# Kernel tuning notes

Hardware: AMD Instinct MI355X
Metric: run time of the kernel (lower is better)

Reference implementation:

```python
import jax, jax.numpy as jnp
import numpy as np

NUM_HEADS = 16
HEAD_DIM = 80
DIM = NUM_HEADS * HEAD_DIM
SEQ = 2048
SCALE = HEAD_DIM ** -0.5


def rotate_half(x):
    x1, x2 = jnp.split(x, 2, axis=-1)
    return jnp.concatenate((-x2, x1), axis=-1)


def setup_inputs() -> dict:
    key = jax.random.key(0)
    ks = jax.random.split(key, 8)
    hidden_states = jax.random.normal(ks[0], (SEQ, DIM), dtype=jnp.float32)
    cu_seqlens = jnp.array([0, SEQ], dtype=jnp.int32)  # unused by the math
    # rotary embeddings for head_dim
    inv_freq = 1.0 / (10000.0 ** (jnp.arange(0, HEAD_DIM // 2, dtype=jnp.float32) / (HEAD_DIM // 2)))
    freqs = jnp.outer(jnp.arange(SEQ, dtype=jnp.float32), inv_freq)  # [S, hd/2]
    emb = jnp.concatenate((freqs, freqs), axis=-1)  # [S, hd]
    cos = jnp.cos(emb)
    sin = jnp.sin(emb)
    w_qkv = jax.random.normal(ks[1], (3 * DIM, DIM), dtype=jnp.float32) * (DIM ** -0.5)
    b_qkv = jax.random.normal(ks[2], (3 * DIM,), dtype=jnp.float32) * 0.02
    w_proj = jax.random.normal(ks[3], (DIM, DIM), dtype=jnp.float32) * (DIM ** -0.5)
    b_proj = jax.random.normal(ks[4], (DIM,), dtype=jnp.float32) * 0.02
    return {"hidden_states": hidden_states, "cu_seqlens": cu_seqlens, "cos": cos,
            "sin": sin, "w_qkv": w_qkv, "b_qkv": b_qkv, "w_proj": w_proj, "b_proj": b_proj}


def reference(hidden_states, cu_seqlens, cos, sin, w_qkv, b_qkv, w_proj, b_proj):
    S = hidden_states.shape[0]
    qkv = hidden_states @ w_qkv.T + b_qkv  # [S, 3*D]
    qkv = qkv.reshape(S, 3, NUM_HEADS, HEAD_DIM)
    q, k, v = qkv[:, 0], qkv[:, 1], qkv[:, 2]  # each [S, H, hd]
    c = cos[:, None, :]  # [S, 1, hd]
    s = sin[:, None, :]
    q = q * c + rotate_half(q) * s
    k = k * c + rotate_half(k) * s
    # SDPA, non-causal: [H, S, S]
    scores = jnp.einsum('shd,thd->hst', q, k) * SCALE
    attn = jax.nn.softmax(scores, axis=-1)
    out = jnp.einsum('hst,thd->shd', attn, v).reshape(S, DIM)
    return out @ w_proj.T + b_proj
```

## Files before the change

kernel.cpp:

```cpp
#include <hip/hip_runtime.h>


#define SEQLEN   2048
#define DIMM     1280
#define NHEADS   16
#define HD       80
#define QKV_N    3840
#define NSPLIT   4
#define KVSPAN   (SEQLEN / NSPLIT)
#define QSCALE_LOG2E 0.16130083587064776f

#define KSTRIDE  88
#define VFSTRIDE 24

#define EXP2F(x) __builtin_amdgcn_exp2f(x)

#define GLD16(gptr, lptr)                                                      \
    __builtin_amdgcn_global_load_lds(                                          \
        (const __attribute__((address_space(1))) void*)(gptr),                 \
        (__attribute__((address_space(3))) void*)(lptr), 16, 0, 0)

typedef float f32x4 __attribute__((ext_vector_type(4)));
typedef _Float16 half8 __attribute__((ext_vector_type(8)));
typedef _Float16 half4 __attribute__((ext_vector_type(4)));
typedef _Float16 half2v __attribute__((ext_vector_type(2)));

static __device__ __forceinline__ f32x4 mfma_16x16x32(half8 a, half8 b, f32x4 c) {
    return __builtin_amdgcn_mfma_f32_16x16x32_f16(a, b, c, 0, 0, 0);
}
static __device__ __forceinline__ f32x4 mfma_16x16x16(half4 a, half4 b, f32x4 c) {
    return __builtin_amdgcn_mfma_f32_16x16x16f16(a, b, c, 0, 0, 0);
}
static __device__ __forceinline__ half4 lo4(half8 v) {
    return __builtin_shufflevector(v, v, 0, 1, 2, 3);
}
static __device__ __forceinline__ half4 hi4(half8 v) {
    return __builtin_shufflevector(v, v, 4, 5, 6, 7);
}

__global__ __launch_bounds__(256)
void cast_all(const float* __restrict__ hs, const float* __restrict__ wq,
              const float* __restrict__ wp, _Float16* __restrict__ dhs,
              _Float16* __restrict__ dwq, _Float16* __restrict__ dwp) {
    const int n1 = SEQLEN * DIMM / 4, n2 = QKV_N * DIMM / 4, n3 = DIMM * DIMM / 4;
    int i = blockIdx.x * 256 + threadIdx.x;
    const float4* src; half4* dst; int j;
    if (i < n1)           { src = (const float4*)hs; dst = (half4*)dhs; j = i; }
    else if (i < n1 + n2) { src = (const float4*)wq; dst = (half4*)dwq; j = i - n1; }
    else if (i < n1 + n2 + n3) { src = (const float4*)wp; dst = (half4*)dwp; j = i - n1 - n2; }
    else return;
    const float4 v = src[j];
    half4 h;
    h.x = (_Float16)v.x; h.y = (_Float16)v.y;
    h.z = (_Float16)v.z; h.w = (_Float16)v.w;
    dst[j] = h;
}

template<bool OUT_F16>
__global__ __launch_bounds__(512, 4)
void gemm_bt128(const _Float16* __restrict__ A, const _Float16* __restrict__ B,
                const float* __restrict__ bias, void* __restrict__ Cout,
                int M, int N, int K) {
    __shared__ __align__(16) _Float16 As[2][128 * 32];
    __shared__ __align__(16) _Float16 Bs[2][128 * 32];
    const int tid  = threadIdx.x;
    const int lane = tid & 63;
    const int wave = tid >> 6;
    const int l15  = lane & 15;
    const int quad = lane >> 4;
    const int wm   = wave & 3;
    const int wn   = wave >> 2;
    const long bm = blockIdx.x, bn = blockIdx.y;

    const _Float16* Ag = A + bm * 128 * (long)K;
    const _Float16* Bg = B + bn * 128 * (long)K;

    const int srow = lane >> 2;
    const int scol = (lane & 3) * 8;
    f32x4 acc[2][4] = {};

    for (int k0 = 0; k0 < K; k0 += 64) {
        __syncthreads();
#pragma unroll
        for (int p = 0; p < 2; p++) {
            const int kp = k0 + p * 32;
            const long r = 16 * wave + srow;
            GLD16(Ag + r * K + kp + scol, &As[p][512 * wave + lane * 8]);
            GLD16(Bg + r * K + kp + scol, &Bs[p][512 * wave + lane * 8]);
        }
        __syncthreads();
#pragma unroll
        for (int p = 0; p < 2; p++) {
            half8 af[2], bf[4];
#pragma unroll
            for (int t = 0; t < 2; t++)
                af[t] = *(const half8*)&As[p][(wm * 32 + t * 16 + l15) * 32 + quad * 8];
#pragma unroll
            for (int t = 0; t < 4; t++)
                bf[t] = *(const half8*)&Bs[p][(wn * 64 + t * 16 + l15) * 32 + quad * 8];
#pragma unroll
            for (int mt = 0; mt < 2; mt++)
#pragma unroll
                for (int nt = 0; nt < 4; nt++)
                    acc[mt][nt] = mfma_16x16x32(af[mt], bf[nt], acc[mt][nt]);
        }
    }

    float bv[4];
#pragma unroll
    for (int nt = 0; nt < 4; nt++)
        bv[nt] = bias[bn * 128 + wn * 64 + nt * 16 + l15];

#pragma unroll
    for (int mt = 0; mt < 2; mt++) {
#pragma unroll
        for (int r = 0; r < 4; r++) {
            const long row = bm * 128 + wm * 32 + mt * 16 + quad * 4 + r;
#pragma unroll
            for (int nt = 0; nt < 4; nt++) {
                const long col = bn * 128 + wn * 64 + nt * 16 + l15;
                const float v = acc[mt][nt][r] + bv[nt];
                if (OUT_F16) ((_Float16*)Cout)[row * (long)N + col] = (_Float16)v;
                else         ((float*)Cout)[row * (long)N + col] = v;
            }
        }
    }
}

template<bool OUT_F16>
__global__ __launch_bounds__(256, 2)
void gemm_bt64(const _Float16* __restrict__ A, const _Float16* __restrict__ B,
               const float* __restrict__ bias, void* __restrict__ Cout,
               int M, int N, int K) {
    __shared__ __align__(16) _Float16 As[2][64 * 32];
    __shared__ __align__(16) _Float16 Bs[2][128 * 32];
    const int tid  = threadIdx.x;
    const int lane = tid & 63;
    const int wave = tid >> 6;
    const int l15  = lane & 15;
    const int quad = lane >> 4;
    const int wm   = wave & 1;
    const int wn   = wave >> 1;
    const long bm = blockIdx.x, bn = blockIdx.y;

    const _Float16* Ag = A + bm * 64 * (long)K;
    const _Float16* Bg = B + bn * 128 * (long)K;

    const int srow = lane >> 2;
    const int scol = (lane & 3) * 8;
    f32x4 acc[2][4] = {};

    for (int k0 = 0; k0 < K; k0 += 64) {
        __syncthreads();
#pragma unroll
        for (int p = 0; p < 2; p++) {
            const int kp = k0 + p * 32;
            const long arow = 16 * wave + srow;
            GLD16(Ag + arow * K + kp + scol, &As[p][512 * wave + lane * 8]);
#pragma unroll
            for (int cc = 0; cc < 2; cc++) {
                const int c = wave + cc * 4;
                const long brow = 16 * c + srow;
                GLD16(Bg + brow * K + kp + scol, &Bs[p][512 * c + lane * 8]);
            }
        }
        __syncthreads();
#pragma unroll
        for (int p = 0; p < 2; p++) {
            half8 af[2], bf[4];
#pragma unroll
            for (int t = 0; t < 2; t++)
                af[t] = *(const half8*)&As[p][(wm * 32 + t * 16 + l15) * 32 + quad * 8];
#pragma unroll
            for (int t = 0; t < 4; t++)
                bf[t] = *(const half8*)&Bs[p][(wn * 64 + t * 16 + l15) * 32 + quad * 8];
#pragma unroll
            for (int mt = 0; mt < 2; mt++)
#pragma unroll
                for (int nt = 0; nt < 4; nt++)
                    acc[mt][nt] = mfma_16x16x32(af[mt], bf[nt], acc[mt][nt]);
        }
    }

    float bv[4];
#pragma unroll
    for (int nt = 0; nt < 4; nt++)
        bv[nt] = bias[bn * 128 + wn * 64 + nt * 16 + l15];

#pragma unroll
    for (int mt = 0; mt < 2; mt++) {
#pragma unroll
        for (int r = 0; r < 4; r++) {
            const long row = bm * 64 + wm * 32 + mt * 16 + quad * 4 + r;
#pragma unroll
            for (int nt = 0; nt < 4; nt++) {
                const long col = bn * 128 + wn * 64 + nt * 16 + l15;
                const float v = acc[mt][nt][r] + bv[nt];
                if (OUT_F16) ((_Float16*)Cout)[row * (long)N + col] = (_Float16)v;
                else         ((float*)Cout)[row * (long)N + col] = v;
            }
        }
    }
}

__global__ __launch_bounds__(256)
void rope_repack_t(const _Float16* __restrict__ qkv,
                   const float* __restrict__ cosb,
                   const float* __restrict__ sinb,
                   _Float16* __restrict__ Qh,
                   _Float16* __restrict__ Kh,
                   _Float16* __restrict__ Vt) {
    const int s0 = blockIdx.x * 64;
    const int h  = blockIdx.y;
    __shared__ __align__(16) _Float16 Ts[64 * 88];
    const int tid = threadIdx.x;

    for (int i = tid; i < 640; i += 256) {
        const int r = i / 10, c = (i - r * 10) * 8;
        *(half8*)&Ts[r * 88 + c] =
            *(const half8*)&qkv[(long)(s0 + r) * QKV_N + 2 * DIMM + h * HD + c];
    }

    for (int i = tid; i < 320; i += 256) {
        const int r = i / 5, d = (i - r * 5) * 8;
        const _Float16* row = qkv + (long)(s0 + r) * QKV_N + h * HD;
        const half8 q0 = *(const half8*)&row[d];
        const half8 q1 = *(const half8*)&row[d + 40];
        const half8 k0 = *(const half8*)&row[DIMM + d];
        const half8 k1 = *(const half8*)&row[DIMM + d + 40];
        const float4 cA = *(const float4*)&cosb[(s0 + r) * HD + d];
        const float4 cB = *(const float4*)&cosb[(s0 + r) * HD + d + 4];
        const float4 sA = *(const float4*)&sinb[(s0 + r) * HD + d];
        const float4 sB = *(const float4*)&sinb[(s0 + r) * HD + d + 4];
        half8 qo0, qo1, ko0, ko1;
#pragma unroll
        for (int j = 0; j < 8; j++) {
            const float cj = (j < 4) ? cA[j] : cB[j - 4];
            const float sj = (j < 4) ? sA[j] : sB[j - 4];
            qo0[j] = (_Float16)(((float)q0[j] * cj - (float)q1[j] * sj) * QSCALE_LOG2E);
            qo1[j] = (_Float16)(((float)q1[j] * cj + (float)q0[j] * sj) * QSCALE_LOG2E);
            ko0[j] = (_Float16)((float)k0[j] * cj - (float)k1[j] * sj);
            ko1[j] = (_Float16)((float)k1[j] * cj + (float)k0[j] * sj);
        }
        const long o = ((long)h * SEQLEN + s0 + r) * HD;
        *(half8*)&Qh[o + d]      = qo0;
        *(half8*)&Qh[o + d + 40] = qo1;
        *(half8*)&Kh[o + d]      = ko0;
        *(half8*)&Kh[o + d + 40] = ko1;
    }
    __syncthreads();
    for (int i = tid; i < 640; i += 256) {
        const int d = i >> 3, sc = (i & 7) * 8;
        half8 v;
#pragma unroll
        for (int j = 0; j < 8; j++) v[j] = Ts[(sc + j) * 88 + d];
        *(half8*)&Vt[((long)h * HD + d) * SEQLEN + s0 + sc] = v;
    }
}

__global__ __launch_bounds__(512, 4)
void attn_kernel(const _Float16* __restrict__ Qh, const _Float16* __restrict__ Kh,
                 const _Float16* __restrict__ Vt,
                 _Float16* __restrict__ Ohat0, _Float16* __restrict__ Ohat1,
                 float* __restrict__ Lpart) {
    const int s0 = blockIdx.x * 256;
    const int h  = blockIdx.y;
    const int z  = blockIdx.z;
    __shared__ __align__(16) _Float16 Ks[64 * KSTRIDE];
    __shared__ __align__(16) _Float16 VF[5 * 64 * VFSTRIDE];

    const int tid  = threadIdx.x;
    const int lane = tid & 63;
    const int wave = tid >> 6;
    const int l15  = lane & 15;
    const int quad = lane >> 4;

    const int zBeg = z * KVSPAN, zEnd = zBeg + KVSPAN;

    const _Float16* Qg0 = Qh + ((long)h * SEQLEN + s0 + wave * 32 + l15) * HD;
    const _Float16* Qg1 = Qg0 + 16 * (long)HD;
    const half8 qA0 = *(const half8*)&Qg0[quad * 8];
    const half8 qA1 = *(const half8*)&Qg0[32 + quad * 8];
    const half4 qA2 = *(const half4*)&Qg0[64 + quad * 4];
    const half8 qB0 = *(const half8*)&Qg1[quad * 8];
    const half8 qB1 = *(const half8*)&Qg1[32 + quad * 8];
    const half4 qB2 = *(const half4*)&Qg1[64 + quad * 4];

    int offA, dsA, offB, dsB0, dsB1 = 0, offC = 0, dsC0 = 0, dsC1 = 0;
    {
        const int rA = tid / 10, cA = (tid - rA * 10) * 8;
        offA = rA * HD + cA;
        dsA  = rA * KSTRIDE + cA;
        if (tid < 128) {
            const int cB = tid + 512;
            const int rB = cB / 10, ccB = (cB - rB * 10) * 8;
            offB = rB * HD + ccB;
            dsB0 = rB * KSTRIDE + ccB;
        } else {
            const int v = tid - 128, d = v >> 3, c8 = (v & 7) * 8;
            offB = d * SEQLEN + c8;
            const int nt = d >> 4, ld = d & 15, ct = c8 >> 4, qb = (c8 & 15) >> 2;
            dsB0 = (nt * 64 + qb * 16 + ld) * VFSTRIDE + ct * 4;
            dsB1 = (nt * 64 + (qb + 1) * 16 + ld) * VFSTRIDE + ct * 4;
        }
        if (tid < 256) {
            const int v = tid + 384, d = v >> 3, c8 = (v & 7) * 8;
            offC = d * SEQLEN + c8;
            const int nt = d >> 4, ld = d & 15, ct = c8 >> 4, qb = (c8 & 15) >> 2;
            dsC0 = (nt * 64 + qb * 16 + ld) * VFSTRIDE + ct * 4;
            dsC1 = (nt * 64 + (qb + 1) * 16 + ld) * VFSTRIDE + ct * 4;
        }
    }
    const _Float16* KzBase = Kh + ((long)h * SEQLEN + zBeg) * HD;
    const _Float16* VzBase = Vt + (long)h * HD * SEQLEN + zBeg;

    f32x4 oaccA[5] = {}, oaccB[5] = {};
    float laA0 = 0.f, laA1 = 0.f, laB0 = 0.f, laB1 = 0.f;
    const half2v ones2 = {(_Float16)1.f, (_Float16)1.f};

    for (int t0 = zBeg; t0 < zEnd; t0 += 64) {
        const _Float16* KzT = KzBase + (long)(t0 - zBeg) * HD;
        const _Float16* VzT = VzBase + (t0 - zBeg);
        const half8 a = *(const half8*)(KzT + offA);
        half8 b;
        if (tid < 128) b = *(const half8*)(KzT + offB);
        else           b = *(const half8*)(VzT + offB);
        half8 cv = {};
        if (tid < 256) cv = *(const half8*)(VzT + offC);

        __syncthreads();
        *(half8*)&Ks[dsA] = a;
        if (tid < 128) { *(half8*)&Ks[dsB0] = b; }
        else {
            *(half4*)&VF[dsB0] = lo4(b);
            *(half4*)&VF[dsB1] = hi4(b);
        }
        if (tid < 256) {
            *(half4*)&VF[dsC0] = lo4(cv);
            *(half4*)&VF[dsC1] = hi4(cv);
        }
        __syncthreads();

        f32x4 saA[4] = {}, saB[4] = {};
        __builtin_amdgcn_s_setprio(1);
#pragma unroll
        for (int ct = 0; ct < 4; ct++) {
            const int kb = (ct * 16 + l15) * KSTRIDE;
            const half8 kf0 = *(const half8*)&Ks[kb + quad * 8];
            const half8 kf1 = *(const half8*)&Ks[kb + 32 + quad * 8];
            const half4 kf2 = *(const half4*)&Ks[kb + 64 + quad * 4];
            saA[ct] = mfma_16x16x32(kf0, qA0, saA[ct]);
            saB[ct] = mfma_16x16x32(kf0, qB0, saB[ct]);
            saA[ct] = mfma_16x16x32(kf1, qA1, saA[ct]);
            saB[ct] = mfma_16x16x32(kf1, qB1, saB[ct]);
            saA[ct] = mfma_16x16x16(kf2, qA2, saA[ct]);
            saB[ct] = mfma_16x16x16(kf2, qB2, saB[ct]);
        }
        __builtin_amdgcn_s_setprio(0);

        half4 pbA[4], pbB[4];
#pragma unroll
        for (int ct = 0; ct < 4; ct++) {
            {
                const float e0 = EXP2F(saA[ct][0]);
                const float e1 = EXP2F(saA[ct][1]);
                const float e2 = EXP2F(saA[ct][2]);
                const float e3 = EXP2F(saA[ct][3]);
                const half2v p01 = __builtin_bit_cast(half2v, __builtin_amdgcn_cvt_pkrtz(e0, e1));
                const half2v p23 = __builtin_bit_cast(half2v, __builtin_amdgcn_cvt_pkrtz(e2, e3));
                laA0 = __builtin_amdgcn_fdot2(p01, ones2, laA0, false);
                laA1 = __builtin_amdgcn_fdot2(p23, ones2, laA1, false);
                pbA[ct] = __builtin_shufflevector(p01, p23, 0, 1, 2, 3);
            }
            {
                const float e0 = EXP2F(saB[ct][0]);
                const float e1 = EXP2F(saB[ct][1]);
                const float e2 = EXP2F(saB[ct][2]);
                const float e3 = EXP2F(saB[ct][3]);
                const half2v p01 = __builtin_bit_cast(half2v, __builtin_amdgcn_cvt_pkrtz(e0, e1));
                const half2v p23 = __builtin_bit_cast(half2v, __builtin_amdgcn_cvt_pkrtz(e2, e3));
                laB0 = __builtin_amdgcn_fdot2(p01, ones2, laB0, false);
                laB1 = __builtin_amdgcn_fdot2(p23, ones2, laB1, false);
                pbB[ct] = __builtin_shufflevector(p01, p23, 0, 1, 2, 3);
            }
        }

        __builtin_amdgcn_s_setprio(1);
#pragma unroll
        for (int nt = 0; nt < 5; nt++) {
            const half8 va = *(const half8*)&VF[(nt * 64 + lane) * VFSTRIDE];
            const half8 vb = *(const half8*)&VF[(nt * 64 + lane) * VFSTRIDE + 8];
            oaccA[nt] = mfma_16x16x16(lo4(va), pbA[0], oaccA[nt]);
            oaccB[nt] = mfma_16x16x16(lo4(va), pbB[0], oaccB[nt]);
            oaccA[nt] = mfma_16x16x16(hi4(va), pbA[1], oaccA[nt]);
            oaccB[nt] = mfma_16x16x16(hi4(va), pbB[1], oaccB[nt]);
            oaccA[nt] = mfma_16x16x16(lo4(vb), pbA[2], oaccA[nt]);
            oaccB[nt] = mfma_16x16x16(lo4(vb), pbB[2], oaccB[nt]);
            oaccA[nt] = mfma_16x16x16(hi4(vb), pbA[3], oaccA[nt]);
            oaccB[nt] = mfma_16x16x16(hi4(vb), pbB[3], oaccB[nt]);
        }
        __builtin_amdgcn_s_setprio(0);
    }

    float lA = laA0 + laA1, lB = laB0 + laB1;
    lA += __shfl_xor(lA, 16); lA += __shfl_xor(lA, 32);
    lB += __shfl_xor(lB, 16); lB += __shfl_xor(lB, 32);
    const float invA = 1.0f / lA, invB = 1.0f / lB;

    _Float16* Oz = (z < 2) ? Ohat0 : Ohat1;
    const long obase = ((long)(z & 1) * NHEADS + h) * SEQLEN;
    const long lbase = ((long)z * NHEADS + h) * SEQLEN;
    const long rowA = s0 + wave * 32 + l15;
    const long rowB = rowA + 16;
#pragma unroll
    for (int nt = 0; nt < 5; nt++) {
        half4 oA, oB;
#pragma unroll
        for (int r = 0; r < 4; r++) {
            oA[r] = (_Float16)(oaccA[nt][r] * invA);
            oB[r] = (_Float16)(oaccB[nt][r] * invB);
        }
        *(half4*)&Oz[(obase + rowA) * HD + nt * 16 + quad * 4] = oA;
        *(half4*)&Oz[(obase + rowB) * HD + nt * 16 + quad * 4] = oB;
    }
    if (quad == 0) {
        Lpart[lbase + rowA] = lA;
        Lpart[lbase + rowB] = lB;
    }
}

__global__ __launch_bounds__(256)
void attn_combine(const _Float16* __restrict__ Ohat0,
                  const _Float16* __restrict__ Ohat1,
                  const float* __restrict__ Lp,
                  _Float16* __restrict__ attnb) {
    const int i = blockIdx.x * 256 + threadIdx.x;
    if (i >= SEQLEN * DIMM / 4) return;
    const int flat = i * 4;
    const int s = flat / DIMM;
    const int rem = flat - s * DIMM;
    const int h = rem / HD;
    const int d = rem - h * HD;
    float l[NSPLIT], lsum = 0.f;
#pragma unroll
    for (int zi = 0; zi < NSPLIT; zi++) {
        l[zi] = Lp[((long)zi * NHEADS + h) * SEQLEN + s];
        lsum += l[zi];
    }
    const float invl = 1.0f / lsum;
    float acc[4] = {0.f, 0.f, 0.f, 0.f};
#pragma unroll
    for (int zi = 0; zi < NSPLIT; zi++) {
        const _Float16* Oz = (zi < 2) ? Ohat0 : Ohat1;
        const long obase = ((long)(zi & 1) * NHEADS + h) * SEQLEN;
        const half4 o = *(const half4*)&Oz[(obase + s) * HD + d];
        const float w = l[zi] * invl;
#pragma unroll
        for (int j = 0; j < 4; j++) acc[j] += (float)o[j] * w;
    }
    half4 o;
#pragma unroll
    for (int j = 0; j < 4; j++) o[j] = (_Float16)acc[j];
    *(half4*)&attnb[(long)s * DIMM + rem] = o;
}

extern "C" void kernel_launch(void* const* d_in, const int* in_sizes, int n_in,
                              void* d_out, int out_size, void* d_ws, size_t ws_size,
                              hipStream_t stream) {
    const float* hs     = (const float*)d_in[0];
    const float* cosb   = (const float*)d_in[2];
    const float* sinb   = (const float*)d_in[3];
    const float* w_qkv  = (const float*)d_in[4];
    const float* b_qkv  = (const float*)d_in[5];
    const float* w_proj = (const float*)d_in[6];
    const float* b_proj = (const float*)d_in[7];
    float* out = (float*)d_out;

    _Float16* hsb    = (_Float16*)d_ws;
    _Float16* wqkvb  = hsb    + (long)SEQLEN * DIMM;
    _Float16* wprojb = wqkvb  + (long)QKV_N * DIMM;
    _Float16* qkv    = wprojb + (long)DIMM * DIMM;
    _Float16* Qh     = qkv    + (long)SEQLEN * QKV_N;
    _Float16* Kh     = Qh     + (long)NHEADS * SEQLEN * HD;
    _Float16* Vtb    = Kh     + (long)NHEADS * SEQLEN * HD;
    _Float16* attnb  = Vtb    + (long)NHEADS * HD * SEQLEN;

    _Float16* Ohat0  = (_Float16*)d_ws;
    float*    LpartB = (float*)(Ohat0 + (long)2 * NHEADS * SEQLEN * HD);
    _Float16* Ohat1  = qkv;

    {
        const int ntot = (SEQLEN * DIMM + QKV_N * DIMM + DIMM * DIMM) / 4;
        cast_all<<<(ntot + 255) / 256, 256, 0, stream>>>(
            hs, w_qkv, w_proj, hsb, wqkvb, wprojb);
    }

    gemm_bt128<true><<<dim3(SEQLEN / 128, QKV_N / 128), 512, 0, stream>>>(
        hsb, wqkvb, b_qkv, qkv, SEQLEN, QKV_N, DIMM);

    rope_repack_t<<<dim3(SEQLEN / 64, NHEADS), 256, 0, stream>>>(
        qkv, cosb, sinb, Qh, Kh, Vtb);

    attn_kernel<<<dim3(SEQLEN / 256, NHEADS, NSPLIT), 512, 0, stream>>>(
        Qh, Kh, Vtb, Ohat0, Ohat1, LpartB);

    attn_combine<<<(SEQLEN * DIMM / 4 + 255) / 256, 256, 0, stream>>>(
        Ohat0, Ohat1, LpartB, attnb);

    gemm_bt64<false><<<dim3(SEQLEN / 64, DIMM / 128), 256, 0, stream>>>(
        attnb, wprojb, b_proj, out, SEQLEN, DIMM, DIMM);
}
```

Measured before the change: 187.6 us.

## Prefetch next K/V tile into registers, widen combine to half8, raise gemm occupancy

The attention loop now loads the next K/V tile from global memory into registers right after the LDS store barrier, so the loads overlap the current tile's MFMA work instead of stalling at the loop top. The split-combine kernel processes 8 halves per thread with 16-byte loads and stores, halving its thread count. The output projection GEMM's launch bounds ask for 4 blocks per SM instead of 2. The prefetch keeps extra registers live, and the launch-bound change may force register spills.

```diff
diff --git a/kernel.cpp b/kernel.cpp
--- a/kernel.cpp
+++ b/kernel.cpp
@@ -128,7 +128,7 @@
 }
 
 template<bool OUT_F16>
-__global__ __launch_bounds__(256, 2)
+__global__ __launch_bounds__(256, 4)
 void gemm_bt64(const _Float16* __restrict__ A, const _Float16* __restrict__ B,
                const float* __restrict__ bias, void* __restrict__ Cout,
                int M, int N, int K) {
@@ -314,32 +314,38 @@
     const _Float16* KzBase = Kh + ((long)h * SEQLEN + zBeg) * HD;
     const _Float16* VzBase = Vt + (long)h * HD * SEQLEN + zBeg;
 
+    half8 sga, sgb, sgc = (half8)(_Float16)0.f;
+    sga = *(const half8*)(KzBase + offA);
+    if (tid < 128) sgb = *(const half8*)(KzBase + offB);
+    else           sgb = *(const half8*)(VzBase + offB);
+    if (tid < 256) sgc = *(const half8*)(VzBase + offC);
+
     f32x4 oaccA[5] = {}, oaccB[5] = {};
     float laA0 = 0.f, laA1 = 0.f, laB0 = 0.f, laB1 = 0.f;
     const half2v ones2 = {(_Float16)1.f, (_Float16)1.f};
 
     for (int t0 = zBeg; t0 < zEnd; t0 += 64) {
-        const _Float16* KzT = KzBase + (long)(t0 - zBeg) * HD;
-        const _Float16* VzT = VzBase + (t0 - zBeg);
-        const half8 a = *(const half8*)(KzT + offA);
-        half8 b;
-        if (tid < 128) b = *(const half8*)(KzT + offB);
-        else           b = *(const half8*)(VzT + offB);
-        half8 cv = {};
-        if (tid < 256) cv = *(const half8*)(VzT + offC);
-
         __syncthreads();
-        *(half8*)&Ks[dsA] = a;
-        if (tid < 128) { *(half8*)&Ks[dsB0] = b; }
+        *(half8*)&Ks[dsA] = sga;
+        if (tid < 128) { *(half8*)&Ks[dsB0] = sgb; }
         else {
-            *(half4*)&VF[dsB0] = lo4(b);
-            *(half4*)&VF[dsB1] = hi4(b);
+            *(half4*)&VF[dsB0] = lo4(sgb);
+            *(half4*)&VF[dsB1] = hi4(sgb);
         }
         if (tid < 256) {
-            *(half4*)&VF[dsC0] = lo4(cv);
-            *(half4*)&VF[dsC1] = hi4(cv);
+            *(half4*)&VF[dsC0] = lo4(sgc);
+            *(half4*)&VF[dsC1] = hi4(sgc);
         }
         __syncthreads();
+
+        if (t0 + 64 < zEnd) {
+            const _Float16* KzT = KzBase + (long)(t0 + 64 - zBeg) * HD;
+            const _Float16* VzT = VzBase + (t0 + 64 - zBeg);
+            sga = *(const half8*)(KzT + offA);
+            if (tid < 128) sgb = *(const half8*)(KzT + offB);
+            else           sgb = *(const half8*)(VzT + offB);
+            if (tid < 256) sgc = *(const half8*)(VzT + offC);
+        }
 
         f32x4 saA[4] = {}, saB[4] = {};
         __builtin_amdgcn_s_setprio(1);
@@ -435,8 +441,8 @@
                   const float* __restrict__ Lp,
                   _Float16* __restrict__ attnb) {
     const int i = blockIdx.x * 256 + threadIdx.x;
-    if (i >= SEQLEN * DIMM / 4) return;
-    const int flat = i * 4;
+    if (i >= SEQLEN * DIMM / 8) return;
+    const int flat = i * 8;
     const int s = flat / DIMM;
     const int rem = flat - s * DIMM;
     const int h = rem / HD;
@@ -448,20 +454,20 @@
         lsum += l[zi];
     }
     const float invl = 1.0f / lsum;
-    float acc[4] = {0.f, 0.f, 0.f, 0.f};
+    float acc[8] = {};
 #pragma unroll
     for (int zi = 0; zi < NSPLIT; zi++) {
         const _Float16* Oz = (zi < 2) ? Ohat0 : Ohat1;
         const long obase = ((long)(zi & 1) * NHEADS + h) * SEQLEN;
-        const half4 o = *(const half4*)&Oz[(obase + s) * HD + d];
+        const half8 o = *(const half8*)&Oz[(obase + s) * HD + d];
         const float w = l[zi] * invl;
 #pragma unroll
-        for (int j = 0; j < 4; j++) acc[j] += (float)o[j] * w;
-    }
-    half4 o;
-#pragma unroll
-    for (int j = 0; j < 4; j++) o[j] = (_Float16)acc[j];
-    *(half4*)&attnb[(long)s * DIMM + rem] = o;
+        for (int j = 0; j < 8; j++) acc[j] += (float)o[j] * w;
+    }
+    half8 o;
+#pragma unroll
+    for (int j = 0; j < 8; j++) o[j] = (_Float16)acc[j];
+    *(half8*)&attnb[(long)s * DIMM + rem] = o;
 }
 
 extern "C" void kernel_launch(void* const* d_in, const int* in_sizes, int n_in,
@@ -504,7 +510,7 @@
     attn_kernel<<<dim3(SEQLEN / 256, NHEADS, NSPLIT), 512, 0, stream>>>(
         Qh, Kh, Vtb, Ohat0, Ohat1, LpartB);
 
-    attn_combine<<<(SEQLEN * DIMM / 4 + 255) / 256, 256, 0, stream>>>(
+    attn_combine<<<(SEQLEN * DIMM / 8 + 255) / 256, 256, 0, stream>>>(
         Ohat0, Ohat1, LpartB, attnb);
 
     gemm_bt64<false><<<dim3(SEQLEN / 64, DIMM / 128), 256, 0, stream>>>(
```

Measured after the change: 188.1 us. Within noise of the previous version (+0.3%).
